# Optimization experiments

Measured on AMD Instinct MI355X. Metric: run time of the kernel, lower is better.

## Reference

```python
import jax, jax.numpy as jnp
import numpy as np

# FP4 E2M1 representable magnitudes (sign handled separately)
_FP4_GRID = np.array([0.0, 0.5, 1.0, 1.5, 2.0, 3.0, 4.0, 6.0], dtype=np.float32)
_FP4_MIDS = (_FP4_GRID[:-1] + _FP4_GRID[1:]) / 2.0  # round-to-nearest boundaries


def fp4_quant_dequant(w):
    """Per-tensor absmax-scaled round-to-nearest FP4 (E2M1) fake quantization."""
    grid = jnp.asarray(_FP4_GRID, dtype=w.dtype)
    mids = jnp.asarray(_FP4_MIDS, dtype=w.dtype)
    scale = jnp.max(jnp.abs(w)) / 6.0  # map absmax -> top FP4 level
    a = jnp.abs(w) / scale
    idx = jnp.searchsorted(mids, a)  # nearest grid index via boundary search
    return grid[idx] * jnp.sign(w) * scale


def fp4_linear(x, W, b):
    # dequantized-weight matmul + bias, as in FP4Linear
    Wq = fp4_quant_dequant(W)
    return x @ Wq.T + b


def setup_inputs() -> dict:
    key = jax.random.key(0)
    k1, k2, k3, k4, k5 = jax.random.split(key, 5)
    B, D_IN, D_H, D_OUT = 8192, 2048, 8192, 2048
    x = jax.random.normal(k1, (B, D_IN), dtype=jnp.float32)
    W1 = jax.random.normal(k2, (D_H, D_IN), dtype=jnp.float32) * 0.02
    b1 = jax.random.normal(k3, (D_H,), dtype=jnp.float32) * 0.02
    W2 = jax.random.normal(k4, (D_OUT, D_H), dtype=jnp.float32) * 0.02
    b2 = jax.random.normal(k5, (D_OUT,), dtype=jnp.float32) * 0.02
    return {"x": x, "W1": W1, "b1": b1, "W2": W2, "b2": b2}


def reference(x, W1, b1, W2, b2):
    h = jax.nn.relu(fp4_linear(x, W1, b1))  # [B, hidden]
    y = fp4_linear(h, W2, b2)                # [B, out]
    return y
```

## Files before the change

kernel.cpp:

```cpp
#include <hip/hip_runtime.h>
#include <hip/hip_bf16.h>
#include <stdint.h>

typedef __attribute__((ext_vector_type(8))) short short8;
typedef __attribute__((ext_vector_type(4))) float f32x4;

#define AS1 __attribute__((address_space(1)))
#define AS3 __attribute__((address_space(3)))

static __device__ __forceinline__ unsigned short f2bf(float f) {
    unsigned int u = __float_as_uint(f);
    u += 0x7FFFu + ((u >> 16) & 1u);
    return (unsigned short)(u >> 16);
}

__global__ void init_amax(unsigned int* amax) {
    if (threadIdx.x < 2) amax[threadIdx.x] = 0u;
}

__global__ void absmax_kernel(const float4* __restrict__ w, size_t n4,
                              unsigned int* __restrict__ out) {
    float m = 0.0f;
    size_t i = (size_t)blockIdx.x * blockDim.x + threadIdx.x;
    size_t stride = (size_t)gridDim.x * blockDim.x;
    for (; i < n4; i += stride) {
        float4 v = w[i];
        m = fmaxf(m, fmaxf(fmaxf(fabsf(v.x), fabsf(v.y)),
                           fmaxf(fabsf(v.z), fabsf(v.w))));
    }
    #pragma unroll
    for (int off = 32; off > 0; off >>= 1)
        m = fmaxf(m, __shfl_down(m, off, 64));
    __shared__ float sm[4];
    int lane = threadIdx.x & 63, wid = threadIdx.x >> 6;
    if (lane == 0) sm[wid] = m;
    __syncthreads();
    if (threadIdx.x == 0) {
        float bm = fmaxf(fmaxf(sm[0], sm[1]), fmaxf(sm[2], sm[3]));
        atomicMax(out, __float_as_uint(bm));
    }
}

static __device__ __forceinline__ unsigned short quant_one(float wv, float scale) {
    float a = fabsf(wv) / scale;
    int idx = (a > 0.25f) + (a > 0.75f) + (a > 1.25f) + (a > 1.75f)
            + (a > 2.5f)  + (a > 3.5f)  + (a > 5.0f);
    const unsigned long long lo = 0x3FC03F803F000000ull;
    const unsigned long long hi = 0x40C0408040404000ull;
    unsigned long long tab = (idx < 4) ? lo : hi;
    unsigned short mag = (unsigned short)(tab >> ((idx & 3) * 16));
    unsigned short sgn = (unsigned short)((__float_as_uint(wv) >> 16) & 0x8000u);
    return (unsigned short)(mag | sgn);
}

__global__ void quant_kernel(const float4* __restrict__ w, size_t n4,
                             const unsigned int* __restrict__ amax,
                             ushort4* __restrict__ q) {
    const float scale = __uint_as_float(*amax) / 6.0f;
    size_t i = (size_t)blockIdx.x * blockDim.x + threadIdx.x;
    size_t stride = (size_t)gridDim.x * blockDim.x;
    for (; i < n4; i += stride) {
        float4 v = w[i];
        ushort4 o;
        o.x = quant_one(v.x, scale);
        o.y = quant_one(v.y, scale);
        o.z = quant_one(v.z, scale);
        o.w = quant_one(v.w, scale);
        q[i] = o;
    }
}

__global__ void cast_bf16_kernel(const float4* __restrict__ x, size_t n4,
                                 ushort4* __restrict__ o) {
    size_t i = (size_t)blockIdx.x * blockDim.x + threadIdx.x;
    size_t stride = (size_t)gridDim.x * blockDim.x;
    for (; i < n4; i += stride) {
        float4 v = x[i];
        ushort4 r;
        r.x = f2bf(v.x); r.y = f2bf(v.y); r.z = f2bf(v.z); r.w = f2bf(v.w);
        o[i] = r;
    }
}


#define GLL(gp, dst)                                                    \
    __builtin_amdgcn_global_load_lds((const AS1 unsigned int*)(gp),     \
        (AS3 unsigned int*)(dst), 16, 0, 0)

#define STGA(gp, ldsoff)                                        \
    do {                                                        \
        GLL((gp) + goffA0, lds + (ldsoff) + tid * 16);          \
        GLL((gp) + goffA1, lds + (ldsoff) + 8192 + tid * 16);   \
    } while (0)

#define STGB(gp, ldsoff)                                        \
    do {                                                        \
        GLL((gp) + goffB0, lds + (ldsoff) + tid * 16);          \
        GLL((gp) + goffB1, lds + (ldsoff) + 8192 + tid * 16);   \
    } while (0)

#define KAB(e) ((size_t)(e) * (LAYA ? 32 : 2))
#define KBB(e) ((size_t)(e) * 2)

#define LD4(dst, base, s0)                                                    \
    do {                                                                      \
        _Pragma("unroll") for (int _i = 0; _i < 4; ++_i)                      \
            dst[_i] = *(const short8*)((base) + ((s0) + _i * 2) * 1024);      \
    } while (0)

#define MFG(AH, ARR, BRR)                                                      \
    do {                                                                       \
        _Pragma("unroll") for (int _i = 0; _i < 4; ++_i)                       \
            _Pragma("unroll") for (int _j = 0; _j < 4; ++_j)                   \
                acc[(AH) * 4 + _i][_j] =                                       \
                    __builtin_amdgcn_mfma_f32_16x16x32_bf16(                   \
                        ARR[_i], BRR[_j], acc[(AH) * 4 + _i][_j], 0, 0, 0);    \
    } while (0)

#define BAR()  __builtin_amdgcn_s_barrier()
#define PRIO(x) __builtin_amdgcn_s_setprio(x)
#define SCHB() __builtin_amdgcn_sched_barrier(0)
#define LGKM(n) do { SCHB(); asm volatile("s_waitcnt lgkmcnt(" #n ")"); SCHB(); } while (0)

#define KTILE(ldsB_, ldsA_, MA1, kA1, oA1, MORE, kNXT, oB0, oB1, oA0, VMODE)   \
    do {                                                                       \
        LD4(bE, ldsB_, 0);                                  \
        LD4(aP, ldsA_, 0);                                     \
        LD4(aQ, ldsA_, 8);                                     \
        if (MA1) STGA(pA1 + KAB(kA1), oA1);                                    \
        LGKM(4);                                \
        PRIO(1); MFG(0, aP, bE); PRIO(0);                                      \
        LD4(bO, ldsB_, 1);                                        \
        LD4(aP, ldsA_, 1);                                     \
        LGKM(8);                               \
        PRIO(1); MFG(1, aQ, bE); PRIO(0);                                      \
        LD4(aQ, ldsA_, 9);                                     \
        LGKM(4);                              \
        PRIO(1); MFG(0, aP, bO); PRIO(0);                                      \
        LGKM(0);                            \
        BAR();                                                                 \
        if (MORE) { STGB(pB0 + KBB(kNXT), oB0); STGB(pB1 + KBB(kNXT), oB1);    \
                    STGA(pA0 + KAB(kNXT), oA0); }                              \
        SCHB();                                                                \
        PRIO(1); MFG(1, aQ, bO); PRIO(0);                                      \
        if (VMODE == 2) { asm volatile("s_waitcnt vmcnt(6)"); }                \
        if (VMODE == 1) { asm volatile("s_waitcnt vmcnt(0)"); }                \
        BAR();                                                                 \
    } while (0)

template <int RELU_BF16, int LAYA>
__global__ __launch_bounds__(512, 2)
void gemm8(const char* __restrict__ A,
           const unsigned short* __restrict__ B,
           const float* __restrict__ bias,
           const unsigned int* __restrict__ amax,
           float* __restrict__ outF,
           char* __restrict__ outH,
           int M, int N, int K, int gx, int cw) {
    __shared__ __align__(16) char lds[131072];

    const int tid  = threadIdx.x;
    const int lane = tid & 63;
    const int wid  = tid >> 6;
    const int wm   = wid >> 2;
    const int wn   = wid & 3;

    const int nwg = gridDim.x;
    const int wg  = blockIdx.x;
    const int c   = wg & 7;
    const int idx = wg >> 3;
    const int nc  = nwg >> 3;
    const int cxc = gx / cw;
    const int ox  = (c % cxc) * cw;
    const int oy  = (c / cxc) * (nc / cw);
    const int bx  = ox + idx % cw;
    const int by  = oy + idx / cw;
    const int col0 = bx * 256;
    const int row0 = by * 256;

    int sp = ((lane & 15) << 6) + ((lane >> 4) << 4);
    sp ^= ((sp >> 9) & 1) << 5;

    const char* ldsA_E = lds + wm * 16384 + sp;
    const char* ldsB_E = lds + 32768 + (wn >> 1) * 16384 + (wn & 1) * 8192 + sp;
    const char* ldsA_O = ldsA_E + 65536;
    const char* ldsB_O = ldsB_E + 65536;

    int goffA0, goffA1, goffB0, goffB1;
    {
        #pragma unroll
        for (int h = 0; h < 2; ++h) {
            int o = h * 8192 + tid * 16;
            int s = o >> 10, b = o & 1023;
            b ^= ((b >> 9) & 1) << 5;
            int row = ((s >> 1) << 4) + (b >> 6);
            int k   = ((s & 1) << 5) + ((b & 63) >> 1);
            int gB  = (row * K + k) * 2;
            int gA  = LAYA ? ((row >> 4) * 262144 + (k >> 4) * 512 +
                              (row & 3) * 128 + ((row >> 2) & 3) * 32 + (k & 15) * 2)
                           : gB;
            if (h == 0) { goffA0 = gA; goffB0 = gB; }
            else        { goffA1 = gA; goffB1 = gB; }
        }
    }
    const char* pA0 = A + (LAYA ? (size_t)row0 * 16384 : (size_t)row0 * K * 2);
    const char* pA1 = A + (LAYA ? (size_t)(row0 + 128) * 16384
                                : (size_t)(row0 + 128) * K * 2);
    const char* pB0 = (const char*)B + (size_t)col0 * K * 2;
    const char* pB1 = (const char*)B + (size_t)(col0 + 128) * K * 2;

    STGB(pB0, 32768); STGB(pB1, 49152); STGA(pA0, 0); STGA(pA1, 16384);
    STGB(pB0 + KBB(64), 98304); STGB(pB1 + KBB(64), 114688);
    STGA(pA0 + KAB(64), 65536);
    asm volatile("s_waitcnt vmcnt(6)");
    BAR();

    f32x4 acc[8][4] = {};
    short8 aP[4], aQ[4], bE[4], bO[4];
    const int NIT = K >> 7;

    for (int it = 0; it < NIT - 1; ++it) {
        const int o0 = it * 128;
        KTILE(ldsB_E, ldsA_E, 1, o0 + 64, 81920,
              1, o0 + 128, 32768, 49152, 0, 2);
        KTILE(ldsB_O, ldsA_O, 1, o0 + 128, 16384,
              1, o0 + 192, 98304, 114688, 65536, 2);
    }
    {
        const int o0 = (NIT - 1) * 128;
        KTILE(ldsB_E, ldsA_E, 1, o0 + 64, 81920,
              0, 0, 0, 0, 0, 1);
        KTILE(ldsB_O, ldsA_O, 0, 0, 0,
              0, 0, 0, 0, 0, 0);
    }

    const float scale = __uint_as_float(*amax) / 6.0f;

    if (RELU_BF16) {
        const int gbit = (lane >> 4) * 32 + (lane & 15) * 2;
        #pragma unroll
        for (int j = 0; j < 4; ++j) {
            const int col = col0 + wn * 64 + j * 16 + (lane & 15);
            const float bvv = bias[col];
            const size_t ktb = (size_t)((col0 >> 4) + wn * 4 + j) * 512;
            #pragma unroll
            for (int i = 0; i < 8; ++i) {
                const size_t rtb = (size_t)(((row0 + wm * 128) >> 4) + i) * 262144;
                #pragma unroll
                for (int r = 0; r < 4; ++r) {
                    float v = fmaxf(acc[i][j][r] * scale + bvv, 0.0f);
                    *(unsigned short*)(outH + rtb + ktb + r * 128 + gbit) = f2bf(v);
                }
            }
        }
    } else {
        #pragma unroll
        for (int p = 0; p < 2; ++p) {
            if (wm == p) {
                #pragma unroll
                for (int j = 0; j < 4; ++j) {
                    const int colb = wn * 64 + j * 16 + (lane & 15);
                    const float bvv = bias[col0 + colb];
                    #pragma unroll
                    for (int i = 0; i < 8; ++i) {
                        #pragma unroll
                        for (int r = 0; r < 4; ++r) {
                            const int row_l = i * 16 + (lane >> 4) * 4 + r;
                            const int blk = (colb >> 2) ^ (((row_l >> 2) & 3) << 2);
                            *(float*)(lds + row_l * 1024 + blk * 16 + (colb & 3) * 4)
                                = acc[i][j][r] * scale + bvv;
                        }
                    }
                }
            }
            asm volatile("s_waitcnt lgkmcnt(0)");
            BAR();
            #pragma unroll
            for (int q = 0; q < 16; ++q) {
                const int flat  = q * 8192 + tid * 16;
                const int row_l = flat >> 10;
                const int blk0  = (flat >> 4) & 63;
                const int blk   = blk0 ^ (((row_l >> 2) & 3) << 2);
                f32x4 v = *(const f32x4*)(lds + row_l * 1024 + blk * 16);
                *(f32x4*)(outF + (size_t)(row0 + p * 128 + row_l) * N
                                 + col0 + blk0 * 4) = v;
            }
            BAR();
        }
    }
}

extern "C" void kernel_launch(void* const* d_in, const int* in_sizes, int n_in,
                              void* d_out, int out_size, void* d_ws, size_t ws_size,
                              hipStream_t stream) {
    const float* x  = (const float*)d_in[0];
    const float* W1 = (const float*)d_in[1];
    const float* b1 = (const float*)d_in[2];
    const float* W2 = (const float*)d_in[3];
    const float* b2 = (const float*)d_in[4];
    float* out = (float*)d_out;

    const int Bm = 8192, Din = 2048, Dh = 8192, Dout = 2048;
    const size_t nW1 = (size_t)Dh * Din;
    const size_t nW2 = (size_t)Dout * Dh;
    const size_t nX  = (size_t)Bm * Din;
    const size_t nH  = (size_t)Bm * Dh;

    const size_t need = 256 + 2 * (nW1 + nW2 + nX + nH);
    if (ws_size < need) return;

    uint8_t* ws = (uint8_t*)d_ws;
    unsigned int*   amax = (unsigned int*)ws;
    unsigned short* Q1 = (unsigned short*)(ws + 256);
    unsigned short* Q2 = Q1 + nW1;
    unsigned short* Xb = Q2 + nW2;
    char*           H  = (char*)(Xb + nX);

    init_amax<<<1, 64, 0, stream>>>(amax);
    absmax_kernel<<<1024, 256, 0, stream>>>((const float4*)W1, nW1 / 4, amax + 0);
    absmax_kernel<<<1024, 256, 0, stream>>>((const float4*)W2, nW2 / 4, amax + 1);
    quant_kernel<<<2048, 256, 0, stream>>>((const float4*)W1, nW1 / 4, amax + 0, (ushort4*)Q1);
    quant_kernel<<<2048, 256, 0, stream>>>((const float4*)W2, nW2 / 4, amax + 1, (ushort4*)Q2);
    cast_bf16_kernel<<<2048, 256, 0, stream>>>((const float4*)x, nX / 4, (ushort4*)Xb);

    gemm8<1, 0><<<dim3((Dh / 256) * (Bm / 256)), 512, 0, stream>>>(
        (const char*)Xb, Q1, b1, amax + 0, nullptr, H,
        Bm, Dh, Din, Dh / 256, 16);
    gemm8<0, 1><<<dim3((Dout / 256) * (Bm / 256)), 512, 0, stream>>>(
        H, Q2, b2, amax + 1, out, nullptr,
        Bm, Dout, Dh, Dout / 256, 8);
}
```

Measured before the change: 534.2 us.

## Restructure GEMM main loop into full-tile double buffering with interleaved LDS reads

```diff
diff --git a/kernel.cpp b/kernel.cpp
--- a/kernel.cpp
+++ b/kernel.cpp
@@ -87,65 +87,63 @@
     __builtin_amdgcn_global_load_lds((const AS1 unsigned int*)(gp),     \
         (AS3 unsigned int*)(dst), 16, 0, 0)
 
-#define STGA(gp, ldsoff)                                        \
-    do {                                                        \
-        GLL((gp) + goffA0, lds + (ldsoff) + tid * 16);          \
-        GLL((gp) + goffA1, lds + (ldsoff) + 8192 + tid * 16);   \
-    } while (0)
-
-#define STGB(gp, ldsoff)                                        \
-    do {                                                        \
-        GLL((gp) + goffB0, lds + (ldsoff) + tid * 16);          \
-        GLL((gp) + goffB1, lds + (ldsoff) + 8192 + tid * 16);   \
-    } while (0)
-
 #define KAB(e) ((size_t)(e) * (LAYA ? 32 : 2))
 #define KBB(e) ((size_t)(e) * 2)
 
-#define LD4(dst, base, s0)                                                    \
-    do {                                                                      \
-        _Pragma("unroll") for (int _i = 0; _i < 4; ++_i)                      \
-            dst[_i] = *(const short8*)((base) + ((s0) + _i * 2) * 1024);      \
-    } while (0)
-
-#define MFG(AH, ARR, BRR)                                                      \
-    do {                                                                       \
-        _Pragma("unroll") for (int _i = 0; _i < 4; ++_i)                       \
-            _Pragma("unroll") for (int _j = 0; _j < 4; ++_j)                   \
-                acc[(AH) * 4 + _i][_j] =                                       \
-                    __builtin_amdgcn_mfma_f32_16x16x32_bf16(                   \
-                        ARR[_i], BRR[_j], acc[(AH) * 4 + _i][_j], 0, 0, 0);    \
-    } while (0)
+#define STAGE_T(kA, kB, bufw)                                           \
+    { GLL(pA0 + (kA) + goffA0, lds + (bufw) + tid * 16);                \
+      GLL(pA0 + (kA) + goffA1, lds + (bufw) + 8192 + tid * 16);         \
+      GLL(pA1 + (kA) + goffA0, lds + (bufw) + 16384 + tid * 16);        \
+      GLL(pA1 + (kA) + goffA1, lds + (bufw) + 24576 + tid * 16);        \
+      GLL(pB0 + (kB) + goffB0, lds + (bufw) + 32768 + tid * 16);        \
+      GLL(pB0 + (kB) + goffB1, lds + (bufw) + 40960 + tid * 16);        \
+      GLL(pB1 + (kB) + goffB0, lds + (bufw) + 49152 + tid * 16);        \
+      GLL(pB1 + (kB) + goffB1, lds + (bufw) + 57344 + tid * 16); }
+
+#define LD4P(dst, base, s0)                                             \
+    { dst[0] = *(const short8*)((base) + (s0) * 1024);                  \
+      dst[1] = *(const short8*)((base) + ((s0) + 2) * 1024);            \
+      dst[2] = *(const short8*)((base) + ((s0) + 4) * 1024);            \
+      dst[3] = *(const short8*)((base) + ((s0) + 6) * 1024); }
+
+#define NOP9 ((void)0)
+
+#define MQ1(AH, I, J, ARR, BRR)                                         \
+    acc[(AH) * 4 + (I)][J] = __builtin_amdgcn_mfma_f32_16x16x32_bf16(   \
+        ARR[I], BRR[J], acc[(AH) * 4 + (I)][J], 0, 0, 0)
 
 #define BAR()  __builtin_amdgcn_s_barrier()
 #define PRIO(x) __builtin_amdgcn_s_setprio(x)
 #define SCHB() __builtin_amdgcn_sched_barrier(0)
 #define LGKM(n) do { SCHB(); asm volatile("s_waitcnt lgkmcnt(" #n ")"); SCHB(); } while (0)
 
-#define KTILE(ldsB_, ldsA_, MA1, kA1, oA1, MORE, kNXT, oB0, oB1, oA0, VMODE)   \
-    do {                                                                       \
-        LD4(bE, ldsB_, 0);                                  \
-        LD4(aP, ldsA_, 0);                                     \
-        LD4(aQ, ldsA_, 8);                                     \
-        if (MA1) STGA(pA1 + KAB(kA1), oA1);                                    \
-        LGKM(4);                                \
-        PRIO(1); MFG(0, aP, bE); PRIO(0);                                      \
-        LD4(bO, ldsB_, 1);                                        \
-        LD4(aP, ldsA_, 1);                                     \
-        LGKM(8);                               \
-        PRIO(1); MFG(1, aQ, bE); PRIO(0);                                      \
-        LD4(aQ, ldsA_, 9);                                     \
-        LGKM(4);                              \
-        PRIO(1); MFG(0, aP, bO); PRIO(0);                                      \
-        LGKM(0);                            \
-        BAR();                                                                 \
-        if (MORE) { STGB(pB0 + KBB(kNXT), oB0); STGB(pB1 + KBB(kNXT), oB1);    \
-                    STGA(pA0 + KAB(kNXT), oA0); }                              \
-        SCHB();                                                                \
-        PRIO(1); MFG(1, aQ, bO); PRIO(0);                                      \
-        if (VMODE == 2) { asm volatile("s_waitcnt vmcnt(6)"); }                \
-        if (VMODE == 1) { asm volatile("s_waitcnt vmcnt(0)"); }                \
-        BAR();                                                                 \
+#define CLUST(AH, ARR, BRR, S1, S2)                                     \
+    { MQ1(AH,0,0,ARR,BRR); MQ1(AH,1,0,ARR,BRR);                         \
+      SCHB(); S1; SCHB();                                               \
+      MQ1(AH,2,0,ARR,BRR); MQ1(AH,3,0,ARR,BRR);                         \
+      MQ1(AH,0,1,ARR,BRR); MQ1(AH,1,1,ARR,BRR);                         \
+      SCHB(); S2; SCHB();                                               \
+      MQ1(AH,2,1,ARR,BRR); MQ1(AH,3,1,ARR,BRR);                         \
+      MQ1(AH,0,2,ARR,BRR); MQ1(AH,1,2,ARR,BRR);                         \
+      MQ1(AH,2,2,ARR,BRR); MQ1(AH,3,2,ARR,BRR);                         \
+      MQ1(AH,0,3,ARR,BRR); MQ1(AH,1,3,ARR,BRR);                         \
+      MQ1(AH,2,3,ARR,BRR); MQ1(AH,3,3,ARR,BRR); }
+
+#define KTILE(ldsAc, ldsBc, STG_STMT, DO_VM, SL1, SL2)                        \
+    do {                                                                      \
+        LGKM(0);      \
+        PRIO(1); CLUST(0, aP, bE, LD4P(aQ, ldsAc, 8), LD4P(bO, ldsBc, 1));    \
+        PRIO(0);                                                              \
+        LGKM(4);                               \
+        PRIO(1); CLUST(1, aQ, bE, LD4P(aP, ldsAc, 1), NOP9); PRIO(0);         \
+        LGKM(0);                                        \
+        PRIO(1); CLUST(0, aP, bO, LD4P(aQ, ldsAc, 9), NOP9); PRIO(0);         \
+        LGKM(0);                       \
+        if (DO_VM) { asm volatile("s_waitcnt vmcnt(0)"); }                    \
+        BAR();           \
+        STG_STMT;                                                             \
+        SCHB();                                                               \
+        PRIO(1); CLUST(1, aQ, bO, SL1, SL2); PRIO(0);                         \
     } while (0)
 
 template <int RELU_BF16, int LAYA>
@@ -209,30 +207,30 @@
     const char* pB0 = (const char*)B + (size_t)col0 * K * 2;
     const char* pB1 = (const char*)B + (size_t)(col0 + 128) * K * 2;
 
-    STGB(pB0, 32768); STGB(pB1, 49152); STGA(pA0, 0); STGA(pA1, 16384);
-    STGB(pB0 + KBB(64), 98304); STGB(pB1 + KBB(64), 114688);
-    STGA(pA0 + KAB(64), 65536);
-    asm volatile("s_waitcnt vmcnt(6)");
-    BAR();
-
     f32x4 acc[8][4] = {};
     short8 aP[4], aQ[4], bE[4], bO[4];
-    const int NIT = K >> 7;
-
-    for (int it = 0; it < NIT - 1; ++it) {
-        const int o0 = it * 128;
-        KTILE(ldsB_E, ldsA_E, 1, o0 + 64, 81920,
-              1, o0 + 128, 32768, 49152, 0, 2);
-        KTILE(ldsB_O, ldsA_O, 1, o0 + 128, 16384,
-              1, o0 + 192, 98304, 114688, 65536, 2);
-    }
-    {
-        const int o0 = (NIT - 1) * 128;
-        KTILE(ldsB_E, ldsA_E, 1, o0 + 64, 81920,
-              0, 0, 0, 0, 0, 1);
-        KTILE(ldsB_O, ldsA_O, 0, 0, 0,
-              0, 0, 0, 0, 0, 0);
-    }
+
+    STAGE_T(0, 0, 0);
+    STAGE_T(KAB(64), KBB(64), 65536);
+    asm volatile("s_waitcnt vmcnt(8)");
+    BAR();
+    LD4P(bE, ldsB_E, 0);
+    LD4P(aP, ldsA_E, 0);
+
+    const int NT = K >> 6;
+    const int NP = NT >> 1;
+
+    for (int p = 0; p < NP - 1; ++p) {
+        const size_t a2 = KAB((size_t)(p * 2 + 2) * 64);
+        const size_t b2 = KBB((size_t)(p * 2 + 2) * 64);
+        KTILE(ldsA_E, ldsB_E, STAGE_T(a2, b2, 0), 1,
+              LD4P(bE, ldsB_O, 0), LD4P(aP, ldsA_O, 0));
+        KTILE(ldsA_O, ldsB_O, STAGE_T(a2 + KAB(64), b2 + KBB(64), 65536), 1,
+              LD4P(bE, ldsB_E, 0), LD4P(aP, ldsA_E, 0));
+    }
+    KTILE(ldsA_E, ldsB_E, NOP9, 1,
+          LD4P(bE, ldsB_O, 0), LD4P(aP, ldsA_O, 0));
+    KTILE(ldsA_O, ldsB_O, NOP9, 0, NOP9, NOP9);
 
     const float scale = __uint_as_float(*amax) / 6.0f;
 
@@ -255,8 +253,8 @@
         }
     } else {
         #pragma unroll
-        for (int p = 0; p < 2; ++p) {
-            if (wm == p) {
+        for (int p2 = 0; p2 < 2; ++p2) {
+            if (wm == p2) {
                 #pragma unroll
                 for (int j = 0; j < 4; ++j) {
                     const int colb = wn * 64 + j * 16 + (lane & 15);
@@ -282,7 +280,7 @@
                 const int blk0  = (flat >> 4) & 63;
                 const int blk   = blk0 ^ (((row_l >> 2) & 3) << 2);
                 f32x4 v = *(const f32x4*)(lds + row_l * 1024 + blk * 16);
-                *(f32x4*)(outF + (size_t)(row0 + p * 128 + row_l) * N
+                *(f32x4*)(outF + (size_t)(row0 + p2 * 128 + row_l) * N
                                  + col0 + blk0 * 4) = v;
             }
             BAR();
```

Measured after the change: 660.9 us. +23.7%, slower.
